# Kernel optimization log

Measured on AMD Instinct MI355X. Metric: run time of the kernel, lower is better.

## Reference

```python
import jax, jax.numpy as jnp
import numpy as np

RADIUS = 3
SIGMA = 2.0
T_STEPS = 30


def _gauss_kernel():
    i = jnp.arange(-RADIUS, RADIUS + 1, dtype=jnp.float32)
    w = jnp.exp(-0.5 * (i / SIGMA) ** 2)
    return w / w.sum()


def _gauss_axis(x, w, axis):
    # scipy mode='reflect' == numpy pad mode='symmetric'
    pad = [(0, 0)] * x.ndim
    pad[axis] = (RADIUS, RADIUS)
    xp = jnp.pad(x, pad, mode='symmetric')
    n = x.shape[axis]
    out = w[0] * jax.lax.slice_in_dim(xp, 0, n, axis=axis)
    for k in range(1, 2 * RADIUS + 1):
        out = out + w[k] * jax.lax.slice_in_dim(xp, k, k + n, axis=axis)
    return out


def _dog(x):
    # scipy gaussian_filter with scalar sigma filters EVERY axis (incl. batch, channel).
    # sigma2=0 axis filters are skipped by scipy -> blurred2 == x.
    w = _gauss_kernel()
    g = x
    for ax in range(x.ndim):
        g = _gauss_axis(g, w, ax)
    return jnp.abs(g - x)


def _conv(x, w):
    return jax.lax.conv_general_dilated(
        x, w, window_strides=(1, 1), padding='VALID',
        dimension_numbers=('NCHW', 'OIHW', 'NCHW'))


def _maxpool2(x, pad):
    return jax.lax.reduce_window(
        x, -jnp.inf, jax.lax.max, (1, 1, 2, 2), (1, 1, 2, 2),
        [(0, 0), (0, 0), (pad, pad), (pad, pad)])


def setup_inputs() -> dict:
    key = jax.random.key(0)
    kx, k1, k2, k3 = jax.random.split(key, 4)
    x = jax.random.uniform(kx, (4096, 1, 28, 28), dtype=jnp.float32)
    # model constructor takes abs() of all conv weights
    w1 = jnp.abs(jax.random.normal(k1, (4, 1, 3, 3), dtype=jnp.float32) / 3.0)
    w2 = jnp.abs(jax.random.normal(k2, (4, 4, 3, 3), dtype=jnp.float32) / 6.0)
    w3 = jnp.abs(jax.random.normal(k3, (1, 4, 3, 3), dtype=jnp.float32) / 6.0)
    return {'x': x, 'w1': w1, 'w2': w2, 'w3': w3}


def reference(x, w1, w2, w3):
    x = x.reshape(-1, 1, 28, 28)
    n = x.shape[0]
    dt = x.dtype
    # DoG preproc + global-max normalization (input is constant across timesteps,
    # so computing it once is mathematically identical to the per-step recompute)
    d = _dog(x)
    d = d / d.max()

    def step(carry, _):
        v1, v2, v3, v4, pred = carry
        # IFNode(4.5): integrate, fire, hard reset to 0
        v1 = v1 + d
        s1 = (v1 >= 4.5).astype(dt)
        v1 = jnp.where(s1 > 0, 0.0, v1)
        # conv1 -> IFNode(4.5) -> maxpool2
        v2 = v2 + _conv(s1, w1)                 # [n,4,26,26]
        s2 = (v2 >= 4.5).astype(dt)
        v2 = jnp.where(s2 > 0, 0.0, v2)
        p1 = _maxpool2(s2, 0)                   # [n,4,13,13]
        # conv2 -> IFNode(1.0) -> maxpool2(pad=1)
        v3 = v3 + _conv(p1, w2)                 # [n,4,11,11]
        s3 = (v3 >= 1.0).astype(dt)
        v3 = jnp.where(s3 > 0, 0.0, v3)
        p2 = _maxpool2(s3, 1)                   # [n,4,6,6]
        # conv3 -> LIFNode(tau=2, v_th=1.0, decay_input=True, hard reset)
        c3 = _conv(p2, w3)                      # [n,1,4,4]
        v4 = v4 + (c3 - v4) / 2.0
        s4 = (v4 >= 1.0).astype(dt)
        v4 = jnp.where(s4 > 0, 0.0, v4)
        return (v1, v2, v3, v4, pred + s4), None

    z = lambda s: jnp.zeros(s, dt)
    carry0 = (z((n, 1, 28, 28)), z((n, 4, 26, 26)), z((n, 4, 11, 11)),
              z((n, 1, 4, 4)), z((n, 1, 4, 4)))
    (v1, v2, v3, v4, pred), _ = jax.lax.scan(step, carry0, None, length=T_STEPS)
    return (pred / T_STEPS).reshape(-1, 4, 4)
```

## Files before the change

### kernel.cpp

```cpp
#include <hip/hip_runtime.h>
#include <math.h>

#define HW 784
#define TSTEPS 30
#define TCHUNK 10

struct GaussW { float w[7]; };

__device__ __forceinline__ float fadd(float a, float b) { return __fadd_rn(a, b); }
__device__ __forceinline__ float fmul(float a, float b) { return __fmul_rn(a, b); }
__device__ __forceinline__ float fsub(float a, float b) { return __fsub_rn(a, b); }

#if defined(__has_builtin)
#  if __has_builtin(__builtin_amdgcn_ubfe)
#    define UBFE(x, o, w) __builtin_amdgcn_ubfe((unsigned)(x), (unsigned)(o), (unsigned)(w))
#  endif
#endif
#ifndef UBFE
#  define UBFE(x, o, w) (((unsigned)(x) >> (o)) & ((1u << (w)) - 1u))
#endif

#define WFENCE() asm volatile("s_waitcnt lgkmcnt(0)" ::: "memory")

__device__ __forceinline__ int refl(int i, int n) {
    if (i < 0) return -i - 1;
    if (i >= n) return 2 * n - 1 - i;
    return i;
}

__device__ void dog_sample(const float* __restrict__ x, int b, int nbatch,
                           const GaussW gw, float* g, float* t,
                           float* dout, int tid) {
    for (int p = tid; p < HW; p += 256) {
        float acc = fmul(gw.w[0], x[(size_t)refl(b - 3, nbatch) * HW + p]);
        #pragma unroll
        for (int k = 1; k < 7; ++k)
            acc = fadd(acc, fmul(gw.w[k], x[(size_t)refl(b - 3 + k, nbatch) * HW + p]));
        float h = fmul(gw.w[0], acc);
        #pragma unroll
        for (int k = 1; k < 7; ++k)
            h = fadd(h, fmul(gw.w[k], acc));
        g[p] = h;
    }
    __syncthreads();
    for (int p = tid; p < HW; p += 256) {
        int i = p / 28, j = p - (p / 28) * 28;
        float acc = fmul(gw.w[0], g[refl(i - 3, 28) * 28 + j]);
        #pragma unroll
        for (int k = 1; k < 7; ++k)
            acc = fadd(acc, fmul(gw.w[k], g[refl(i - 3 + k, 28) * 28 + j]));
        t[p] = acc;
    }
    __syncthreads();
    for (int p = tid; p < HW; p += 256) {
        int i = p / 28, j = p - (p / 28) * 28;
        float acc = fmul(gw.w[0], t[i * 28 + refl(j - 3, 28)]);
        #pragma unroll
        for (int k = 1; k < 7; ++k)
            acc = fadd(acc, fmul(gw.w[k], t[i * 28 + refl(j - 3 + k, 28)]));
        dout[p] = fabsf(fsub(acc, x[(size_t)b * HW + p]));
    }
    __syncthreads();
}

__global__ void init_kernel(unsigned int* dmax) { *dmax = 0u; }

template<bool CACHE>
__global__ __launch_bounds__(256) void dmax_kernel(const float* __restrict__ x,
                                                   int nbatch, GaussW gw,
                                                   unsigned int* __restrict__ dmax,
                                                   float* __restrict__ dcache) {
    __shared__ float gS[4][HW];
    __shared__ float tS[4][HW];
    int tid = threadIdx.x;
    int lane = tid & 63, wv = tid >> 6;
    int b = blockIdx.x * 4 + wv;
    int bs = b < nbatch ? b : nbatch - 1;
    float* g = gS[wv];
    float* t = tS[wv];
    const float* xb = x + (size_t)bs * HW;
    const float* xr[7];
    #pragma unroll
    for (int k = 0; k < 7; ++k)
        xr[k] = x + (size_t)refl(bs - 3 + k, nbatch) * HW;

    for (int r = 0; r < 13; ++r) {
        int p = (r << 6) + lane;
        if (p < HW) {
            float acc = fmul(gw.w[0], xr[0][p]);
            #pragma unroll
            for (int k = 1; k < 7; ++k)
                acc = fadd(acc, fmul(gw.w[k], xr[k][p]));
            float h = fmul(gw.w[0], acc);
            #pragma unroll
            for (int k = 1; k < 7; ++k)
                h = fadd(h, fmul(gw.w[k], acc));
            g[p] = h;
        }
    }
    WFENCE();
    for (int r = 0; r < 13; ++r) {
        int p = (r << 6) + lane;
        if (p < HW) {
            int i = p / 28, j = p - (p / 28) * 28;
            float acc = fmul(gw.w[0], g[refl(i - 3, 28) * 28 + j]);
            #pragma unroll
            for (int k = 1; k < 7; ++k)
                acc = fadd(acc, fmul(gw.w[k], g[refl(i - 3 + k, 28) * 28 + j]));
            t[p] = acc;
        }
    }
    WFENCE();
    float mx = 0.f;
    for (int r = 0; r < 13; ++r) {
        int p = (r << 6) + lane;
        if (p < HW) {
            int i = p / 28, j = p - (p / 28) * 28;
            float acc = fmul(gw.w[0], t[i * 28 + refl(j - 3, 28)]);
            #pragma unroll
            for (int k = 1; k < 7; ++k)
                acc = fadd(acc, fmul(gw.w[k], t[i * 28 + refl(j - 3 + k, 28)]));
            float d = fabsf(fsub(acc, xb[p]));
            if (CACHE) dcache[(size_t)bs * HW + p] = d;
            mx = fmaxf(mx, d);
        }
    }
    #pragma unroll
    for (int off = 32; off; off >>= 1) mx = fmaxf(mx, __shfl_down(mx, off, 64));
    if (lane == 0) atomicMax(dmax, __float_as_uint(mx));
}

template<bool CACHE>
__global__ __launch_bounds__(256, 6) void sim_kernel(const float* __restrict__ x,
        int nbatch,
        const float* __restrict__ w1g, const float* __restrict__ w2g,
        const float* __restrict__ w3g, GaussW gw,
        const unsigned int* __restrict__ dmaxp,
        const float* __restrict__ dcache,
        float* __restrict__ out) {
    __shared__ __align__(16) float4 lut[512];
    __shared__ __align__(8)  float2 lut2[768];
    __shared__ float lut3[96];
    __shared__ float wts[216];
    __shared__ unsigned s1m[TCHUNK * 28];
    __shared__ __align__(8) unsigned p1p[TCHUNK * 26];
    __shared__ unsigned p2p[TCHUNK * 6];

    int tid = threadIdx.x;
    int b = blockIdx.x;
    if (b >= nbatch) b = nbatch - 1;

    if (tid < 36)  wts[tid]       = w1g[tid];
    if (tid < 144) wts[36 + tid]  = w2g[tid];
    if (tid < 36)  wts[180 + tid] = w3g[tid];

    float dmaxv = __uint_as_float(*dmaxp);
    float dnr[4];
    if (CACHE) {
        const float* dcb = dcache + (size_t)b * HW;
        #pragma unroll
        for (int k = 0; k < 4; ++k) {
            int p = tid + (k << 8);
            dnr[k] = (p < HW) ? __fdiv_rn(dcb[p], dmaxv) : 0.f;
        }
    } else {
        float* scr = (float*)lut;
        dog_sample(x, b, nbatch, gw, scr, scr + HW, scr, tid);
        #pragma unroll
        for (int k = 0; k < 4; ++k) {
            int p = tid + (k << 8);
            dnr[k] = (p < HW) ? __fdiv_rn(scr[p], dmaxv) : 0.f;
        }
    }
    __syncthreads();

    for (int e = tid; e < 512; e += 256) {
        float a0 = 0.f, a1 = 0.f, a2 = 0.f, a3 = 0.f;
        #pragma unroll
        for (int k = 0; k < 9; ++k) {
            bool bit = (e >> k) & 1;
            a0 = fadd(a0, bit ? wts[k]      : 0.0f);
            a1 = fadd(a1, bit ? wts[9 + k]  : 0.0f);
            a2 = fadd(a2, bit ? wts[18 + k] : 0.0f);
            a3 = fadd(a3, bit ? wts[27 + k] : 0.0f);
        }
        lut[e] = make_float4(a0, a1, a2, a3);
    }
    for (int e = tid; e < 768; e += 256) {
        int rowIdx = e >> 4, idx = e & 15;
        int cout = rowIdx / 12, rem = rowIdx - cout * 12;
        int ic = rem / 3, ki = rem - ic * 3;
        const float* wb = &wts[36 + cout * 36 + ic * 9 + ki * 3];
        float xx = 0.f, yy = 0.f;
        #pragma unroll
        for (int kk = 0; kk < 3; ++kk) {
            xx = fadd(xx, ((idx >> kk) & 1) ? wb[kk] : 0.0f);
            yy = fadd(yy, ((idx >> (kk + 1)) & 1) ? wb[kk] : 0.0f);
        }
        lut2[e] = make_float2(xx, yy);
    }
    if (tid < 96) {
        int ric = tid >> 3, idx = tid & 7;
        int ic = ric / 3, ki = ric - ic * 3;
        const float* wb = &wts[180 + ic * 9 + ki * 3];
        float xx = 0.f;
        #pragma unroll
        for (int kk = 0; kk < 3; ++kk)
            xx = fadd(xx, ((idx >> kk) & 1) ? wb[kk] : 0.0f);
        lut3[tid] = xx;
    }
    #pragma unroll
    for (int j = 0; j < 3; ++j) {
        int idx = tid + (j << 8);
        if (idx < 600) {
            if (idx < 280) s1m[idx] = 0u;
            else if (idx < 540) p1p[idx - 280] = 0u;
            else p2p[idx - 540] = 0u;
        }
    }
    __syncthreads();

    int l1w_[4]; unsigned l1b_[4];
    #pragma unroll
    for (int k = 0; k < 4; ++k) {
        int e = tid + (k << 8); if (e >= HW) e = 0;
        int rw = e / 28;
        l1w_[k] = rw; l1b_[k] = 1u << (e - rw * 28);
    }
    bool okq = tid < 169;
    int qq1 = okq ? tid : 0;
    int pi1 = qq1 / 13, pj1 = qq1 - pi1 * 13;
    int sr1 = 2 * pi1; unsigned sh1 = (unsigned)(2 * pj1);
    unsigned pb1 = 1u << (pj1 + 1);
    bool hasB = tid >= 248;
    int i2cA, lb2A, p2wA; unsigned js2A, shA, b20A, b21A;
    int i2cB, lb2B, p2wB; unsigned js2B, shB, b20B, b21B;
    {
        int m = tid;
        int row = m / 6, sub = m - row * 6;
        int j0 = (sub < 5) ? 2 * sub : 10;
        int c = row / 11, i2 = row - c * 11;
        i2cA = i2; js2A = (unsigned)(j0 + 1) + ((unsigned)(c & 1) << 4);
        lb2A = c * 192; shA = 6u * (unsigned)c;
        p2wA = (i2 + 1) >> 1;
        b20A = 1u << (j0 >> 1);
        b21A = (sub < 5) ? (2u << (j0 >> 1)) : 0u;
        int wA = c >> 1; i2cA = i2cA * 2 + wA;
        i2cA = i2;
        m = hasB ? 256 + (tid - 248) : 0;
        row = m / 6; sub = m - row * 6;
        j0 = (sub < 5) ? 2 * sub : 10;
        c = row / 11; i2 = row - c * 11;
        i2cB = i2; js2B = (unsigned)(j0 + 1) + ((unsigned)(c & 1) << 4);
        lb2B = c * 192; shB = 6u * (unsigned)c;
        p2wB = (i2 + 1) >> 1;
        b20B = 1u << (j0 >> 1);
        b21B = (sub < 5) ? (2u << (j0 >> 1)) : 0u;
    }
    int cwA = 0, cwB = 0;
    { int m = tid; int row = m / 6; cwA = (row / 11) >> 1; }
    { int m = hasB ? 256 + (tid - 248) : 0; int row = m / 6; cwB = (row / 11) >> 1; }
    int rr3 = (tid >> 2) & 3, cc3 = tid & 3;

    float v2q[16] = {};
    float v3A[2] = {0.f, 0.f}, v3B[2] = {0.f, 0.f};
    float v1m[4] = {};
    float v4 = 0.f, pred = 0.f;

    #pragma unroll 1
    for (int c = 0; c < TSTEPS / TCHUNK; ++c) {
        #pragma unroll 1
        for (int tt = 0; tt < TCHUNK; ++tt) {
            unsigned* s1 = s1m + tt * 28;
            #pragma unroll
            for (int k = 0; k < 4; ++k) {
                if (k < 3 || tid < 16) {
                    float v = fadd(v1m[k], dnr[k]);
                    bool spk = v >= 4.5f;
                    v1m[k] = spk ? 0.f : v;
                    if (spk) atomicOr(&s1[l1w_[k]], l1b_[k]);
                }
            }
        }
        __syncthreads();

        if (okq) {
            #pragma unroll 1
            for (int tt = 0; tt < TCHUNK; ++tt) {
                const unsigned* s1 = s1m + tt * 28;
                unsigned m0 = s1[sr1], m1 = s1[sr1 + 1], m2 = s1[sr1 + 2], m3 = s1[sr1 + 3];
                unsigned a = UBFE(m0, sh1, 4), bq = UBFE(m1, sh1, 4),
                         cq = UBFE(m2, sh1, 4), dq = UBFE(m3, sh1, 4);
                unsigned a7 = a & 7u, b7 = bq & 7u, c7 = cq & 7u, d7 = dq & 7u;
                unsigned a1 = a >> 1, b1 = bq >> 1, c1 = cq >> 1, d1 = dq >> 1;
                unsigned p00 = a7 | (b7 << 3) | (c7 << 6);
                unsigned p01 = a1 | (b1 << 3) | (c1 << 6);
                unsigned p10 = b7 | (c7 << 3) | (d7 << 6);
                unsigned p11 = b1 | (c1 << 3) | (d1 << 6);
                float4 e00 = lut[p00], e01 = lut[p01], e10 = lut[p10], e11 = lut[p11];
                unsigned cb0 = 0, cb1 = 0, cb2 = 0, cb3 = 0;
                #define C1U(E, ci) { float v; bool s; \
                    v = fadd(v2q[(ci)*4+0], E.x); s = v>=4.5f; v2q[(ci)*4+0] = s?0.f:v; cb0 |= (unsigned)s; \
                    v = fadd(v2q[(ci)*4+1], E.y); s = v>=4.5f; v2q[(ci)*4+1] = s?0.f:v; cb1 |= (unsigned)s; \
                    v = fadd(v2q[(ci)*4+2], E.z); s = v>=4.5f; v2q[(ci)*4+2] = s?0.f:v; cb2 |= (unsigned)s; \
                    v = fadd(v2q[(ci)*4+3], E.w); s = v>=4.5f; v2q[(ci)*4+3] = s?0.f:v; cb3 |= (unsigned)s; }
                C1U(e00, 0) C1U(e01, 1) C1U(e10, 2) C1U(e11, 3)
                #undef C1U
                unsigned* pw = &p1p[(tt * 13 + pi1) * 2];
                unsigned orm0 = (cb0 ? pb1 : 0u) | (cb1 ? (pb1 << 16) : 0u);
                unsigned orm1 = (cb2 ? pb1 : 0u) | (cb3 ? (pb1 << 16) : 0u);
                if (orm0) atomicOr(&pw[0], orm0);
                if (orm1) atomicOr(&pw[1], orm1);
            }
        } else {
            int idx = tid - 169;
            if (idx < TCHUNK * 6) p2p[idx] = 0u;
        }
        __syncthreads();

        #pragma unroll 1
        for (int tt = 0; tt < TCHUNK; ++tt) {
            const uint2* pp = (const uint2*)&p1p[tt * 26];
            unsigned* p2w = &p2p[tt * 6];
            {
                uint2 r0 = pp[i2cA], r1 = pp[i2cA + 1], r2 = pp[i2cA + 2];
                float accA = 0.f, accB = 0.f;
                #pragma unroll
                for (int ic = 0; ic < 4; ++ic) {
                    unsigned w0 = (cwA == 0) ? ((ic < 2) ? r0.x : r0.y)
                                             : ((ic < 2) ? r0.x : r0.y);
                    unsigned rw0 = (ic < 2) ? r0.x : r0.y;
                    unsigned rw1 = (ic < 2) ? r1.x : r1.y;
                    unsigned rw2 = (ic < 2) ? r2.x : r2.y;
                    unsigned fo = (unsigned)(js2A & 15u) + ((unsigned)(ic & 1) << 4);
                    (void)w0;
                    #pragma unroll
                    for (int ki = 0; ki < 3; ++ki) {
                        unsigned row = (ki == 0) ? rw0 : (ki == 1) ? rw1 : rw2;
                        unsigned idx = UBFE(row, fo, 4);
                        float2 e = lut2[lb2A + (ic * 3 + ki) * 16 + idx];
                        accA = fadd(accA, e.x);
                        accB = fadd(accB, e.y);
                    }
                }
                float va = fadd(v3A[0], accA);
                float vb = fadd(v3A[1], accB);
                bool sa = va >= 1.0f, sb = vb >= 1.0f;
                v3A[0] = sa ? 0.f : va; v3A[1] = sb ? 0.f : vb;
                unsigned orm = (sa ? b20A : 0u) | (sb ? b21A : 0u);
                if (orm) atomicOr(&p2w[p2wA], orm << shA);
            }
            if (hasB) {
                uint2 r0 = pp[i2cB], r1 = pp[i2cB + 1], r2 = pp[i2cB + 2];
                float accA = 0.f, accB = 0.f;
                #pragma unroll
                for (int ic = 0; ic < 4; ++ic) {
                    unsigned rw0 = (ic < 2) ? r0.x : r0.y;
                    unsigned rw1 = (ic < 2) ? r1.x : r1.y;
                    unsigned rw2 = (ic < 2) ? r2.x : r2.y;
                    unsigned fo = (unsigned)(js2B & 15u) + ((unsigned)(ic & 1) << 4);
                    #pragma unroll
                    for (int ki = 0; ki < 3; ++ki) {
                        unsigned row = (ki == 0) ? rw0 : (ki == 1) ? rw1 : rw2;
                        unsigned idx = UBFE(row, fo, 4);
                        float2 e = lut2[lb2B + (ic * 3 + ki) * 16 + idx];
                        accA = fadd(accA, e.x);
                        accB = fadd(accB, e.y);
                    }
                }
                float va = fadd(v3B[0], accA);
                float vb = fadd(v3B[1], accB);
                bool sa = va >= 1.0f, sb = vb >= 1.0f;
                v3B[0] = sa ? 0.f : va; v3B[1] = sb ? 0.f : vb;
                unsigned orm = (sa ? b20B : 0u) | (sb ? b21B : 0u);
                if (orm) atomicOr(&p2w[p2wB], orm << shB);
            }
        }
        __syncthreads();

        if (tid < 16) {
            #pragma unroll 1
            for (int tt = 0; tt < TCHUNK; ++tt) {
                const unsigned* p2 = &p2p[tt * 6];
                unsigned r0 = p2[rr3], r1 = p2[rr3 + 1], r2 = p2[rr3 + 2];
                float acc = 0.f;
                #pragma unroll
                for (int ic = 0; ic < 4; ++ic) {
                    #pragma unroll
                    for (int ki = 0; ki < 3; ++ki) {
                        unsigned row = (ki == 0) ? r0 : (ki == 1) ? r1 : r2;
                        unsigned idx = UBFE(row, 6 * ic + cc3, 3);
                        acc = fadd(acc, lut3[(ic * 3 + ki) * 8 + idx]);
                    }
                }
                v4 = fadd(v4, fmul(fsub(acc, v4), 0.5f));
                if (v4 >= 1.0f) { pred += 1.f; v4 = 0.f; }
            }
        } else {
            #pragma unroll
            for (int j = 0; j < 3; ++j) {
                int idx = (tid - 16) + 240 * j;
                if (idx < 540) {
                    if (idx < 280) s1m[idx] = 0u;
                    else p1p[idx - 280] = 0u;
                }
            }
        }
        __syncthreads();
    }

    if (tid < 16 && blockIdx.x < (unsigned)nbatch)
        out[(size_t)blockIdx.x * 16 + tid] = __fdiv_rn(pred, 30.0f);
}

extern "C" void kernel_launch(void* const* d_in, const int* in_sizes, int n_in,
                              void* d_out, int out_size, void* d_ws, size_t ws_size,
                              hipStream_t stream) {
    const float* x  = (const float*)d_in[0];
    const float* w1 = (const float*)d_in[1];
    const float* w2 = (const float*)d_in[2];
    const float* w3 = (const float*)d_in[3];
    float* out = (float*)d_out;
    unsigned int* dmax = (unsigned int*)d_ws;
    float* dcache = (float*)((char*)d_ws + 16);

    int nbatch = in_sizes[0] / HW;
    size_t need = 16 + (size_t)nbatch * HW * sizeof(float);
    bool cache = ws_size >= need;
    int g4 = (nbatch + 3) / 4;

    GaussW gw;
    {
        float fw[7];
        for (int k = 0; k < 7; ++k) {
            float iv = (float)(k - 3);
            float q = iv / 2.0f;
            float e = -0.5f * (q * q);
            fw[k] = (float)exp((double)e);
        }
        float s = 0.0f;
        for (int k = 0; k < 7; ++k) s += fw[k];
        for (int k = 0; k < 7; ++k) gw.w[k] = fw[k] / s;
    }

    hipLaunchKernelGGL(init_kernel, dim3(1), dim3(1), 0, stream, dmax);
    if (cache) {
        hipLaunchKernelGGL(dmax_kernel<true>, dim3(g4), dim3(256), 0, stream,
                           x, nbatch, gw, dmax, dcache);
        hipLaunchKernelGGL(sim_kernel<true>, dim3(nbatch), dim3(256), 0, stream,
                           x, nbatch, w1, w2, w3, gw, dmax, dcache, out);
    } else {
        hipLaunchKernelGGL(dmax_kernel<false>, dim3(g4), dim3(256), 0, stream,
                           x, nbatch, gw, dmax, dcache);
        hipLaunchKernelGGL(sim_kernel<false>, dim3(nbatch), dim3(256), 0, stream,
                           x, nbatch, w1, w2, w3, gw, dmax, dcache, out);
    }
}
```

Before: 273.2 us.

## Process all timesteps per layer in one pass and build spike masks with wave ballots

The timestep chunking (three chunks of ten) is removed. Spike-mask buffers are sized for all 30 steps, so each layer runs over every timestep with a single barrier between layers, and the per-chunk barriers and buffer clears go away. Layer-1 spikes are now assigned two image rows per wave and packed with __ballot plus direct stores instead of per-thread LDS atomicOr. The cost is more shared memory per block, which may lower occupancy under the launch bounds.

```diff
diff --git a/kernel.cpp b/kernel.cpp
--- a/kernel.cpp
+++ b/kernel.cpp
@@ -3,7 +3,6 @@
 
 #define HW 784
 #define TSTEPS 30
-#define TCHUNK 10
 
 struct GaussW { float w[7]; };
 
@@ -142,11 +141,12 @@
     __shared__ __align__(8)  float2 lut2[768];
     __shared__ float lut3[96];
     __shared__ float wts[216];
-    __shared__ unsigned s1m[TCHUNK * 28];
-    __shared__ __align__(8) unsigned p1p[TCHUNK * 26];
-    __shared__ unsigned p2p[TCHUNK * 6];
+    __shared__ unsigned s1m[TSTEPS * 28];
+    __shared__ __align__(8) unsigned p1p[TSTEPS * 26];
+    __shared__ unsigned p2p[TSTEPS * 6];
 
     int tid = threadIdx.x;
+    int lane = tid & 63, wv = tid >> 6;
     int b = blockIdx.x;
     if (b >= nbatch) b = nbatch - 1;
 
@@ -160,16 +160,20 @@
         const float* dcb = dcache + (size_t)b * HW;
         #pragma unroll
         for (int k = 0; k < 4; ++k) {
-            int p = tid + (k << 8);
-            dnr[k] = (p < HW) ? __fdiv_rn(dcb[p], dmaxv) : 0.f;
+            int r = wv + 4 * k;
+            int p = 56 * r + (lane < 56 ? lane : 0);
+            float d = (r < 14) ? dcb[p] : 0.f;
+            dnr[k] = (lane < 56 && r < 14) ? __fdiv_rn(d, dmaxv) : 0.f;
         }
     } else {
         float* scr = (float*)lut;
         dog_sample(x, b, nbatch, gw, scr, scr + HW, scr, tid);
         #pragma unroll
         for (int k = 0; k < 4; ++k) {
-            int p = tid + (k << 8);
-            dnr[k] = (p < HW) ? __fdiv_rn(scr[p], dmaxv) : 0.f;
+            int r = wv + 4 * k;
+            int p = 56 * r + (lane < 56 ? lane : 0);
+            float d = (r < 14) ? scr[p] : 0.f;
+            dnr[k] = (lane < 56 && r < 14) ? __fdiv_rn(d, dmaxv) : 0.f;
         }
     }
     __syncthreads();
@@ -210,56 +214,42 @@
         lut3[tid] = xx;
     }
     #pragma unroll
-    for (int j = 0; j < 3; ++j) {
+    for (int j = 0; j < 8; ++j) {
         int idx = tid + (j << 8);
-        if (idx < 600) {
-            if (idx < 280) s1m[idx] = 0u;
-            else if (idx < 540) p1p[idx - 280] = 0u;
-            else p2p[idx - 540] = 0u;
-        }
-    }
-    __syncthreads();
-
-    int l1w_[4]; unsigned l1b_[4];
-    #pragma unroll
-    for (int k = 0; k < 4; ++k) {
-        int e = tid + (k << 8); if (e >= HW) e = 0;
-        int rw = e / 28;
-        l1w_[k] = rw; l1b_[k] = 1u << (e - rw * 28);
-    }
+        if (idx < TSTEPS * 60) {
+            if (idx < TSTEPS * 28) s1m[idx] = 0u;
+            else if (idx < TSTEPS * 54) p1p[idx - TSTEPS * 28] = 0u;
+            else p2p[idx - TSTEPS * 54] = 0u;
+        }
+    }
+    __syncthreads();
+
     bool okq = tid < 169;
     int qq1 = okq ? tid : 0;
     int pi1 = qq1 / 13, pj1 = qq1 - pi1 * 13;
     int sr1 = 2 * pi1; unsigned sh1 = (unsigned)(2 * pj1);
     unsigned pb1 = 1u << (pj1 + 1);
     bool hasB = tid >= 248;
-    int i2cA, lb2A, p2wA; unsigned js2A, shA, b20A, b21A;
-    int i2cB, lb2B, p2wB; unsigned js2B, shB, b20B, b21B;
+    int i2A, lbA, pwA; unsigned jsA, shA, bA0, bA1;
+    int i2B, lbB, pwB; unsigned jsB, shB, bB0, bB1;
     {
         int m = tid;
         int row = m / 6, sub = m - row * 6;
         int j0 = (sub < 5) ? 2 * sub : 10;
         int c = row / 11, i2 = row - c * 11;
-        i2cA = i2; js2A = (unsigned)(j0 + 1) + ((unsigned)(c & 1) << 4);
-        lb2A = c * 192; shA = 6u * (unsigned)c;
-        p2wA = (i2 + 1) >> 1;
-        b20A = 1u << (j0 >> 1);
-        b21A = (sub < 5) ? (2u << (j0 >> 1)) : 0u;
-        int wA = c >> 1; i2cA = i2cA * 2 + wA;
-        i2cA = i2;
+        i2A = i2; jsA = (unsigned)(j0 + 1); lbA = c * 192; shA = 6u * (unsigned)c;
+        pwA = (i2 + 1) >> 1;
+        bA0 = 1u << (j0 >> 1);
+        bA1 = (sub < 5) ? (2u << (j0 >> 1)) : 0u;
         m = hasB ? 256 + (tid - 248) : 0;
         row = m / 6; sub = m - row * 6;
         j0 = (sub < 5) ? 2 * sub : 10;
         c = row / 11; i2 = row - c * 11;
-        i2cB = i2; js2B = (unsigned)(j0 + 1) + ((unsigned)(c & 1) << 4);
-        lb2B = c * 192; shB = 6u * (unsigned)c;
-        p2wB = (i2 + 1) >> 1;
-        b20B = 1u << (j0 >> 1);
-        b21B = (sub < 5) ? (2u << (j0 >> 1)) : 0u;
-    }
-    int cwA = 0, cwB = 0;
-    { int m = tid; int row = m / 6; cwA = (row / 11) >> 1; }
-    { int m = hasB ? 256 + (tid - 248) : 0; int row = m / 6; cwB = (row / 11) >> 1; }
+        i2B = i2; jsB = (unsigned)(j0 + 1); lbB = c * 192; shB = 6u * (unsigned)c;
+        pwB = (i2 + 1) >> 1;
+        bB0 = 1u << (j0 >> 1);
+        bB1 = (sub < 5) ? (2u << (j0 >> 1)) : 0u;
+    }
     int rr3 = (tid >> 2) & 3, cc3 = tid & 3;
 
     float v2q[16] = {};
@@ -268,149 +258,132 @@
     float v4 = 0.f, pred = 0.f;
 
     #pragma unroll 1
-    for (int c = 0; c < TSTEPS / TCHUNK; ++c) {
+    for (int tt = 0; tt < TSTEPS; ++tt) {
+        unsigned* s1 = s1m + tt * 28;
+        #pragma unroll
+        for (int k = 0; k < 4; ++k) {
+            if (k < 3 || wv < 2) {
+                int r = wv + 4 * k;
+                float v = fadd(v1m[k], dnr[k]);
+                bool spk = (lane < 56) && (v >= 4.5f);
+                v1m[k] = spk ? 0.f : v;
+                unsigned long long bal = __ballot(spk);
+                if (lane < 2)
+                    s1[2 * r + lane] = (unsigned)(lane ? (bal >> 28) : bal) & 0x0FFFFFFFu;
+            }
+        }
+    }
+    __syncthreads();
+
+    if (okq) {
         #pragma unroll 1
-        for (int tt = 0; tt < TCHUNK; ++tt) {
-            unsigned* s1 = s1m + tt * 28;
-            #pragma unroll
-            for (int k = 0; k < 4; ++k) {
-                if (k < 3 || tid < 16) {
-                    float v = fadd(v1m[k], dnr[k]);
-                    bool spk = v >= 4.5f;
-                    v1m[k] = spk ? 0.f : v;
-                    if (spk) atomicOr(&s1[l1w_[k]], l1b_[k]);
+        for (int tt = 0; tt < TSTEPS; ++tt) {
+            const unsigned* s1 = s1m + tt * 28;
+            unsigned m0 = s1[sr1], m1 = s1[sr1 + 1], m2 = s1[sr1 + 2], m3 = s1[sr1 + 3];
+            unsigned a = UBFE(m0, sh1, 4), bq = UBFE(m1, sh1, 4),
+                     cq = UBFE(m2, sh1, 4), dq = UBFE(m3, sh1, 4);
+            unsigned a7 = a & 7u, b7 = bq & 7u, c7 = cq & 7u, d7 = dq & 7u;
+            unsigned a1 = a >> 1, b1 = bq >> 1, c1 = cq >> 1, d1 = dq >> 1;
+            unsigned p00 = a7 | (b7 << 3) | (c7 << 6);
+            unsigned p01 = a1 | (b1 << 3) | (c1 << 6);
+            unsigned p10 = b7 | (c7 << 3) | (d7 << 6);
+            unsigned p11 = b1 | (c1 << 3) | (d1 << 6);
+            float4 e00 = lut[p00], e01 = lut[p01], e10 = lut[p10], e11 = lut[p11];
+            unsigned cb0 = 0, cb1 = 0, cb2 = 0, cb3 = 0;
+            #define C1U(E, ci) { float v; bool s; \
+                v = fadd(v2q[(ci)*4+0], E.x); s = v>=4.5f; v2q[(ci)*4+0] = s?0.f:v; cb0 |= (unsigned)s; \
+                v = fadd(v2q[(ci)*4+1], E.y); s = v>=4.5f; v2q[(ci)*4+1] = s?0.f:v; cb1 |= (unsigned)s; \
+                v = fadd(v2q[(ci)*4+2], E.z); s = v>=4.5f; v2q[(ci)*4+2] = s?0.f:v; cb2 |= (unsigned)s; \
+                v = fadd(v2q[(ci)*4+3], E.w); s = v>=4.5f; v2q[(ci)*4+3] = s?0.f:v; cb3 |= (unsigned)s; }
+            C1U(e00, 0) C1U(e01, 1) C1U(e10, 2) C1U(e11, 3)
+            #undef C1U
+            unsigned* pw = &p1p[(tt * 13 + pi1) * 2];
+            unsigned orm0 = (cb0 ? pb1 : 0u) | (cb1 ? (pb1 << 16) : 0u);
+            unsigned orm1 = (cb2 ? pb1 : 0u) | (cb3 ? (pb1 << 16) : 0u);
+            if (orm0) atomicOr(&pw[0], orm0);
+            if (orm1) atomicOr(&pw[1], orm1);
+        }
+    }
+    __syncthreads();
+
+    #pragma unroll 1
+    for (int tt = 0; tt < TSTEPS; ++tt) {
+        const uint2* pp = (const uint2*)&p1p[tt * 26];
+        unsigned* p2w = &p2p[tt * 6];
+        {
+            uint2 r0 = pp[i2A], r1 = pp[i2A + 1], r2 = pp[i2A + 2];
+            float accA = 0.f, accB = 0.f;
+            #pragma unroll
+            for (int ic = 0; ic < 4; ++ic) {
+                unsigned rw0 = (ic < 2) ? r0.x : r0.y;
+                unsigned rw1 = (ic < 2) ? r1.x : r1.y;
+                unsigned rw2 = (ic < 2) ? r2.x : r2.y;
+                unsigned fo = jsA + ((unsigned)(ic & 1) << 4);
+                #pragma unroll
+                for (int ki = 0; ki < 3; ++ki) {
+                    unsigned row = (ki == 0) ? rw0 : (ki == 1) ? rw1 : rw2;
+                    unsigned idx = UBFE(row, fo, 4);
+                    float2 e = lut2[lbA + (ic * 3 + ki) * 16 + idx];
+                    accA = fadd(accA, e.x);
+                    accB = fadd(accB, e.y);
                 }
             }
-        }
-        __syncthreads();
-
-        if (okq) {
-            #pragma unroll 1
-            for (int tt = 0; tt < TCHUNK; ++tt) {
-                const unsigned* s1 = s1m + tt * 28;
-                unsigned m0 = s1[sr1], m1 = s1[sr1 + 1], m2 = s1[sr1 + 2], m3 = s1[sr1 + 3];
-                unsigned a = UBFE(m0, sh1, 4), bq = UBFE(m1, sh1, 4),
-                         cq = UBFE(m2, sh1, 4), dq = UBFE(m3, sh1, 4);
-                unsigned a7 = a & 7u, b7 = bq & 7u, c7 = cq & 7u, d7 = dq & 7u;
-                unsigned a1 = a >> 1, b1 = bq >> 1, c1 = cq >> 1, d1 = dq >> 1;
-                unsigned p00 = a7 | (b7 << 3) | (c7 << 6);
-                unsigned p01 = a1 | (b1 << 3) | (c1 << 6);
-                unsigned p10 = b7 | (c7 << 3) | (d7 << 6);
-                unsigned p11 = b1 | (c1 << 3) | (d1 << 6);
-                float4 e00 = lut[p00], e01 = lut[p01], e10 = lut[p10], e11 = lut[p11];
-                unsigned cb0 = 0, cb1 = 0, cb2 = 0, cb3 = 0;
-                #define C1U(E, ci) { float v; bool s; \
-                    v = fadd(v2q[(ci)*4+0], E.x); s = v>=4.5f; v2q[(ci)*4+0] = s?0.f:v; cb0 |= (unsigned)s; \
-                    v = fadd(v2q[(ci)*4+1], E.y); s = v>=4.5f; v2q[(ci)*4+1] = s?0.f:v; cb1 |= (unsigned)s; \
-                    v = fadd(v2q[(ci)*4+2], E.z); s = v>=4.5f; v2q[(ci)*4+2] = s?0.f:v; cb2 |= (unsigned)s; \
-                    v = fadd(v2q[(ci)*4+3], E.w); s = v>=4.5f; v2q[(ci)*4+3] = s?0.f:v; cb3 |= (unsigned)s; }
-                C1U(e00, 0) C1U(e01, 1) C1U(e10, 2) C1U(e11, 3)
-                #undef C1U
-                unsigned* pw = &p1p[(tt * 13 + pi1) * 2];
-                unsigned orm0 = (cb0 ? pb1 : 0u) | (cb1 ? (pb1 << 16) : 0u);
-                unsigned orm1 = (cb2 ? pb1 : 0u) | (cb3 ? (pb1 << 16) : 0u);
-                if (orm0) atomicOr(&pw[0], orm0);
-                if (orm1) atomicOr(&pw[1], orm1);
-            }
-        } else {
-            int idx = tid - 169;
-            if (idx < TCHUNK * 6) p2p[idx] = 0u;
-        }
-        __syncthreads();
-
-        #pragma unroll 1
-        for (int tt = 0; tt < TCHUNK; ++tt) {
-            const uint2* pp = (const uint2*)&p1p[tt * 26];
-            unsigned* p2w = &p2p[tt * 6];
-            {
-                uint2 r0 = pp[i2cA], r1 = pp[i2cA + 1], r2 = pp[i2cA + 2];
-                float accA = 0.f, accB = 0.f;
+            float va = fadd(v3A[0], accA);
+            float vb = fadd(v3A[1], accB);
+            bool sa = va >= 1.0f, sb = vb >= 1.0f;
+            v3A[0] = sa ? 0.f : va; v3A[1] = sb ? 0.f : vb;
+            unsigned orm = (sa ? bA0 : 0u) | (sb ? bA1 : 0u);
+            if (orm) atomicOr(&p2w[pwA], orm << shA);
+        }
+        if (hasB) {
+            uint2 r0 = pp[i2B], r1 = pp[i2B + 1], r2 = pp[i2B + 2];
+            float accA = 0.f, accB = 0.f;
+            #pragma unroll
+            for (int ic = 0; ic < 4; ++ic) {
+                unsigned rw0 = (ic < 2) ? r0.x : r0.y;
+                unsigned rw1 = (ic < 2) ? r1.x : r1.y;
+                unsigned rw2 = (ic < 2) ? r2.x : r2.y;
+                unsigned fo = jsB + ((unsigned)(ic & 1) << 4);
                 #pragma unroll
-                for (int ic = 0; ic < 4; ++ic) {
-                    unsigned w0 = (cwA == 0) ? ((ic < 2) ? r0.x : r0.y)
-                                             : ((ic < 2) ? r0.x : r0.y);
-                    unsigned rw0 = (ic < 2) ? r0.x : r0.y;
-                    unsigned rw1 = (ic < 2) ? r1.x : r1.y;
-                    unsigned rw2 = (ic < 2) ? r2.x : r2.y;
-                    unsigned fo = (unsigned)(js2A & 15u) + ((unsigned)(ic & 1) << 4);
-                    (void)w0;
-                    #pragma unroll
-                    for (int ki = 0; ki < 3; ++ki) {
-                        unsigned row = (ki == 0) ? rw0 : (ki == 1) ? rw1 : rw2;
-                        unsigned idx = UBFE(row, fo, 4);
-                        float2 e = lut2[lb2A + (ic * 3 + ki) * 16 + idx];
-                        accA = fadd(accA, e.x);
-                        accB = fadd(accB, e.y);
-                    }
-                }
-                float va = fadd(v3A[0], accA);
-                float vb = fadd(v3A[1], accB);
-                bool sa = va >= 1.0f, sb = vb >= 1.0f;
-                v3A[0] = sa ? 0.f : va; v3A[1] = sb ? 0.f : vb;
-                unsigned orm = (sa ? b20A : 0u) | (sb ? b21A : 0u);
-                if (orm) atomicOr(&p2w[p2wA], orm << shA);
-            }
-            if (hasB) {
-                uint2 r0 = pp[i2cB], r1 = pp[i2cB + 1], r2 = pp[i2cB + 2];
-                float accA = 0.f, accB = 0.f;
-                #pragma unroll
-                for (int ic = 0; ic < 4; ++ic) {
-                    unsigned rw0 = (ic < 2) ? r0.x : r0.y;
-                    unsigned rw1 = (ic < 2) ? r1.x : r1.y;
-                    unsigned rw2 = (ic < 2) ? r2.x : r2.y;
-                    unsigned fo = (unsigned)(js2B & 15u) + ((unsigned)(ic & 1) << 4);
-                    #pragma unroll
-                    for (int ki = 0; ki < 3; ++ki) {
-                        unsigned row = (ki == 0) ? rw0 : (ki == 1) ? rw1 : rw2;
-                        unsigned idx = UBFE(row, fo, 4);
-                        float2 e = lut2[lb2B + (ic * 3 + ki) * 16 + idx];
-                        accA = fadd(accA, e.x);
-                        accB = fadd(accB, e.y);
-                    }
-                }
-                float va = fadd(v3B[0], accA);
-                float vb = fadd(v3B[1], accB);
-                bool sa = va >= 1.0f, sb = vb >= 1.0f;
-                v3B[0] = sa ? 0.f : va; v3B[1] = sb ? 0.f : vb;
-                unsigned orm = (sa ? b20B : 0u) | (sb ? b21B : 0u);
-                if (orm) atomicOr(&p2w[p2wB], orm << shB);
-            }
-        }
-        __syncthreads();
-
-        if (tid < 16) {
-            #pragma unroll 1
-            for (int tt = 0; tt < TCHUNK; ++tt) {
-                const unsigned* p2 = &p2p[tt * 6];
-                unsigned r0 = p2[rr3], r1 = p2[rr3 + 1], r2 = p2[rr3 + 2];
-                float acc = 0.f;
-                #pragma unroll
-                for (int ic = 0; ic < 4; ++ic) {
-                    #pragma unroll
-                    for (int ki = 0; ki < 3; ++ki) {
-                        unsigned row = (ki == 0) ? r0 : (ki == 1) ? r1 : r2;
-                        unsigned idx = UBFE(row, 6 * ic + cc3, 3);
-                        acc = fadd(acc, lut3[(ic * 3 + ki) * 8 + idx]);
-                    }
-                }
-                v4 = fadd(v4, fmul(fsub(acc, v4), 0.5f));
-                if (v4 >= 1.0f) { pred += 1.f; v4 = 0.f; }
-            }
-        } else {
-            #pragma unroll
-            for (int j = 0; j < 3; ++j) {
-                int idx = (tid - 16) + 240 * j;
-                if (idx < 540) {
-                    if (idx < 280) s1m[idx] = 0u;
-                    else p1p[idx - 280] = 0u;
+                for (int ki = 0; ki < 3; ++ki) {
+                    unsigned row = (ki == 0) ? rw0 : (ki == 1) ? rw1 : rw2;
+                    unsigned idx = UBFE(row, fo, 4);
+                    float2 e = lut2[lbB + (ic * 3 + ki) * 16 + idx];
+                    accA = fadd(accA, e.x);
+                    accB = fadd(accB, e.y);
                 }
             }
-        }
-        __syncthreads();
-    }
-
-    if (tid < 16 && blockIdx.x < (unsigned)nbatch)
-        out[(size_t)blockIdx.x * 16 + tid] = __fdiv_rn(pred, 30.0f);
+            float va = fadd(v3B[0], accA);
+            float vb = fadd(v3B[1], accB);
+            bool sa = va >= 1.0f, sb = vb >= 1.0f;
+            v3B[0] = sa ? 0.f : va; v3B[1] = sb ? 0.f : vb;
+            unsigned orm = (sa ? bB0 : 0u) | (sb ? bB1 : 0u);
+            if (orm) atomicOr(&p2w[pwB], orm << shB);
+        }
+    }
+    __syncthreads();
+
+    if (tid < 16) {
+        #pragma unroll 1
+        for (int tt = 0; tt < TSTEPS; ++tt) {
+            const unsigned* p2 = &p2p[tt * 6];
+            unsigned r0 = p2[rr3], r1 = p2[rr3 + 1], r2 = p2[rr3 + 2];
+            float acc = 0.f;
+            #pragma unroll
+            for (int ic = 0; ic < 4; ++ic) {
+                #pragma unroll
+                for (int ki = 0; ki < 3; ++ki) {
+                    unsigned row = (ki == 0) ? r0 : (ki == 1) ? r1 : r2;
+                    unsigned idx = UBFE(row, 6 * ic + cc3, 3);
+                    acc = fadd(acc, lut3[(ic * 3 + ki) * 8 + idx]);
+                }
+            }
+            v4 = fadd(v4, fmul(fsub(acc, v4), 0.5f));
+            if (v4 >= 1.0f) { pred += 1.f; v4 = 0.f; }
+        }
+        if (blockIdx.x < (unsigned)nbatch)
+            out[(size_t)blockIdx.x * 16 + tid] = __fdiv_rn(pred, 30.0f);
+    }
 }
 
 extern "C" void kernel_launch(void* const* d_in, const int* in_sizes, int n_in,
```

Result: faster. 230.6 us (-15.6%).
